# Kernel tuning notes

Hardware: AMD Instinct MI355X
Metric: run time of the kernel (lower is better)

## Reference

```python
import jax, jax.numpy as jnp
import numpy as np

N, D = 16384, 16
EPS = 1e-15
SQRT_C = 1.0            # curvature c = 1 Poincare ball
MAX_NORM = (1.0 - 1e-5) / SQRT_C
ATANH_CLIP = 1.0 - 1e-7


def _proj(x):
    # clip points to stay strictly inside the Poincare ball
    norm = jnp.maximum(jnp.linalg.norm(x, axis=-1, keepdims=True), EPS)
    scale = jnp.where(norm > MAX_NORM, MAX_NORM / norm, 1.0)
    return x * scale


def _logmap0(x):
    # log map at the origin: artanh(sqrt(c)|x|) * x / (sqrt(c)|x|)
    norm = jnp.maximum(jnp.linalg.norm(x, axis=-1, keepdims=True), EPS)
    arg = jnp.minimum(SQRT_C * norm, ATANH_CLIP)
    return jnp.arctanh(arg) * x / (SQRT_C * norm)


def _expmap0(u):
    # exp map at the origin: tanh(sqrt(c)|u|) * u / (sqrt(c)|u|)
    norm = jnp.maximum(jnp.linalg.norm(u, axis=-1, keepdims=True), EPS)
    return jnp.tanh(SQRT_C * norm) * u / (SQRT_C * norm)


def setup_inputs() -> dict:
    key = jax.random.key(0)
    kx, ka = jax.random.split(key)
    # node embeddings strictly inside the unit ball
    x = 0.3 * jax.random.normal(kx, (N, D), dtype=jnp.float32)
    x = _proj(x)
    # dense non-negative adjacency, row-normalized (mean aggregation)
    adj = jax.random.uniform(ka, (N, N), dtype=jnp.float32)
    adj = adj / jnp.sum(adj, axis=-1, keepdims=True)
    return {"x": x, "adj": adj}


def reference(x, adj):
    x_tangent = _logmap0(x)                 # [N, D] pointwise transcendental
    res = jnp.matmul(adj, x_tangent)        # [N, N] @ [N, D] aggregation
    return _proj(_expmap0(res))             # map back to manifold + project
```

## Files before the change

kernel.cpp:

```cpp
#include <hip/hip_runtime.h>
#include <math.h>

#define NROWS 16384
#define DIM   16
#define KC    512
#define NCH   (NROWS / KC)
#define WGT   256
#define RPW   8
#define RPWG  32
#define NT4   (NROWS / 4)

typedef float vfloat4 __attribute__((ext_vector_type(4)));

static __device__ __forceinline__ void fma4(float4& a, float s, const float4& b) {
    a.x = fmaf(s, b.x, a.x);
    a.y = fmaf(s, b.y, a.y);
    a.z = fmaf(s, b.z, a.z);
    a.w = fmaf(s, b.w, a.w);
}
static __device__ __forceinline__ float dot4(const float4& a) {
    return a.x * a.x + a.y * a.y + a.z * a.z + a.w * a.w;
}
static __device__ __forceinline__ float4 scale4(const float4& a, float s) {
    return make_float4(a.x * s, a.y * s, a.z * s, a.w * s);
}

__global__ void hyp_logmap0(const float* __restrict__ x, float4* __restrict__ xtp) {
    int tid = blockIdx.x * blockDim.x + threadIdx.x;
    int s = tid >> 12;
    int t = tid & (NT4 - 1);
    int row = 4 * t + s;
    const float4* src = (const float4*)(x + (size_t)row * DIM);
    float4 q0 = src[0], q1 = src[1], q2 = src[2], q3 = src[3];
    float n2 = dot4(q0) + dot4(q1) + dot4(q2) + dot4(q3);
    float n  = fmaxf(sqrtf(n2), 1e-15f);
    float arg = fminf(n, 1.0f - 1e-7f);
    float f = atanhf(arg) / n;
    xtp[(0 * 4 + s) * NT4 + t] = scale4(q0, f);
    xtp[(1 * 4 + s) * NT4 + t] = scale4(q1, f);
    xtp[(2 * 4 + s) * NT4 + t] = scale4(q2, f);
    xtp[(3 * 4 + s) * NT4 + t] = scale4(q3, f);
}

__global__ __launch_bounds__(WGT, 2) void hyp_agg(
        const float* __restrict__ adj, const float4* __restrict__ xtp,
        float* __restrict__ out) {
    __shared__ float4 planes[2][16][KC / 4];

    const int tid  = threadIdx.x;
    const int lane = tid & 63;
    const int wave = tid >> 6;
    const int rowBase = blockIdx.x * RPWG + wave * RPW;

    const float* a[RPW];
#pragma unroll
    for (int r = 0; r < RPW; ++r)
        a[r] = adj + (size_t)(rowBase + r) * NROWS;

    float4 acc[RPW][4];
#pragma unroll
    for (int r = 0; r < RPW; ++r)
#pragma unroll
        for (int j = 0; j < 4; ++j)
            acc[r][j] = make_float4(0.f, 0.f, 0.f, 0.f);

    auto stage = [&](int buf, int kc) {
#pragma unroll
        for (int i = 0; i < 8; ++i) {
            const int idx = wave * 8 + i;
            const int p   = idx >> 1;
            const int h   = idx & 1;
            const float4* src = xtp + (size_t)p * NT4 + (kc >> 2) + h * 64 + lane;
            __builtin_amdgcn_global_load_lds(
                (const __attribute__((address_space(1))) void*)src,
                (__attribute__((address_space(3))) void*)&planes[buf][p][h * 64],
                16, 0, 0);
        }
    };

    stage(0, 0);
    __syncthreads();

    for (int c = 0; c < NCH; ++c) {
        const int kc  = c * KC;
        const int buf = c & 1;
        if (c + 1 < NCH) stage(buf ^ 1, kc + KC);

#pragma unroll
        for (int it = 0; it < KC / 256; ++it) {
            const int col = kc + it * 256 + 4 * lane;
            vfloat4 v[RPW];
#pragma unroll
            for (int r = 0; r < RPW; ++r)
                v[r] = __builtin_nontemporal_load((const vfloat4*)(a[r] + col));
#pragma unroll
            for (int s = 0; s < 4; ++s) {
                const int t = it * 64 + lane;
                float4 q0 = planes[buf][0 * 4 + s][t];
                float4 q1 = planes[buf][1 * 4 + s][t];
                float4 q2 = planes[buf][2 * 4 + s][t];
                float4 q3 = planes[buf][3 * 4 + s][t];
#pragma unroll
                for (int r = 0; r < RPW; ++r) {
                    float cr = v[r][s];
                    fma4(acc[r][0], cr, q0);
                    fma4(acc[r][1], cr, q1);
                    fma4(acc[r][2], cr, q2);
                    fma4(acc[r][3], cr, q3);
                }
            }
        }
        __syncthreads();
    }

#pragma unroll
    for (int r = 0; r < RPW; ++r) {
#pragma unroll
        for (int j = 0; j < 4; ++j) {
            float4 vv = acc[r][j];
#pragma unroll
            for (int m = 1; m < 64; m <<= 1) {
                vv.x += __shfl_xor(vv.x, m, 64);
                vv.y += __shfl_xor(vv.y, m, 64);
                vv.z += __shfl_xor(vv.z, m, 64);
                vv.w += __shfl_xor(vv.w, m, 64);
            }
            acc[r][j] = vv;
        }
    }

#pragma unroll
    for (int r = 0; r < RPW; ++r) {
        float4 s0 = acc[r][0], s1 = acc[r][1], s2 = acc[r][2], s3 = acc[r][3];
        float n2 = dot4(s0) + dot4(s1) + dot4(s2) + dot4(s3);
        float n  = fmaxf(sqrtf(n2), 1e-15f);
        float t  = tanhf(n);
        float fac = t / n;
        float ny  = fmaxf(t, 1e-15f);
        const float MAX_NORM = 1.0f - 1e-5f;
        float sc  = (ny > MAX_NORM) ? (MAX_NORM / ny) : 1.0f;
        float tot = fac * sc;
        if (lane == 0) {
            float4* dst = (float4*)(out + (size_t)(rowBase + r) * DIM);
            dst[0] = scale4(s0, tot);
            dst[1] = scale4(s1, tot);
            dst[2] = scale4(s2, tot);
            dst[3] = scale4(s3, tot);
        }
    }
}

extern "C" void kernel_launch(void* const* d_in, const int* in_sizes, int n_in,
                              void* d_out, int out_size, void* d_ws, size_t ws_size,
                              hipStream_t stream) {
    const float* x   = (const float*)d_in[0];
    const float* adj = (const float*)d_in[1];
    float* out  = (float*)d_out;
    float4* xtp = (float4*)d_ws;

    hipLaunchKernelGGL(hyp_logmap0, dim3(NROWS / 256), dim3(256), 0, stream, x, xtp);
    hipLaunchKernelGGL(hyp_agg, dim3(NROWS / RPWG), dim3(WGT), 0, stream, adj, xtp, out);
}
```

Before: 248.1 us.

## Store tangent vectors as bf16 and read them directly from global memory

After: 308.9 us. 24.5% more time.

```diff
diff --git a/kernel.cpp b/kernel.cpp
--- a/kernel.cpp
+++ b/kernel.cpp
@@ -1,14 +1,14 @@
 #include <hip/hip_runtime.h>
+#include <hip/hip_bf16.h>
 #include <math.h>
 
 #define NROWS 16384
 #define DIM   16
-#define KC    512
-#define NCH   (NROWS / KC)
-#define WGT   256
-#define RPW   8
+#define WGT   512
+#define RPW   4
 #define RPWG  32
 #define NT4   (NROWS / 4)
+#define NIT   (NROWS / 256)
 
 typedef float vfloat4 __attribute__((ext_vector_type(4)));
 
@@ -24,29 +24,42 @@
 static __device__ __forceinline__ float4 scale4(const float4& a, float s) {
     return make_float4(a.x * s, a.y * s, a.z * s, a.w * s);
 }
+static __device__ __forceinline__ unsigned short bf16r(float v) {
+    union { float f; unsigned u; } c; c.f = v;
+    unsigned r = c.u + 0x7fffu + ((c.u >> 16) & 1u);
+    return (unsigned short)(r >> 16);
+}
+static __device__ __forceinline__ float bf2f(unsigned short h) {
+    union { unsigned u; float f; } c; c.u = ((unsigned)h) << 16;
+    return c.f;
+}
+static __device__ __forceinline__ float4 unpack4(const ushort4& b) {
+    return make_float4(bf2f(b.x), bf2f(b.y), bf2f(b.z), bf2f(b.w));
+}
 
-__global__ void hyp_logmap0(const float* __restrict__ x, float4* __restrict__ xtp) {
+__global__ void hyp_logmap0(const float* __restrict__ x, ushort4* __restrict__ xtb) {
     int tid = blockIdx.x * blockDim.x + threadIdx.x;
     int s = tid >> 12;
     int t = tid & (NT4 - 1);
     int row = 4 * t + s;
     const float4* src = (const float4*)(x + (size_t)row * DIM);
-    float4 q0 = src[0], q1 = src[1], q2 = src[2], q3 = src[3];
-    float n2 = dot4(q0) + dot4(q1) + dot4(q2) + dot4(q3);
+    float4 q[4] = {src[0], src[1], src[2], src[3]};
+    float n2 = dot4(q[0]) + dot4(q[1]) + dot4(q[2]) + dot4(q[3]);
     float n  = fmaxf(sqrtf(n2), 1e-15f);
     float arg = fminf(n, 1.0f - 1e-7f);
     float f = atanhf(arg) / n;
-    xtp[(0 * 4 + s) * NT4 + t] = scale4(q0, f);
-    xtp[(1 * 4 + s) * NT4 + t] = scale4(q1, f);
-    xtp[(2 * 4 + s) * NT4 + t] = scale4(q2, f);
-    xtp[(3 * 4 + s) * NT4 + t] = scale4(q3, f);
+#pragma unroll
+    for (int j = 0; j < 4; ++j) {
+        float4 sq = scale4(q[j], f);
+        ushort4 b;
+        b.x = bf16r(sq.x); b.y = bf16r(sq.y); b.z = bf16r(sq.z); b.w = bf16r(sq.w);
+        xtb[(j * 4 + s) * NT4 + t] = b;
+    }
 }
 
-__global__ __launch_bounds__(WGT, 2) void hyp_agg(
-        const float* __restrict__ adj, const float4* __restrict__ xtp,
+__global__ __launch_bounds__(WGT, 4) void hyp_agg(
+        const float* __restrict__ adj, const ushort4* __restrict__ xtb,
         float* __restrict__ out) {
-    __shared__ float4 planes[2][16][KC / 4];
-
     const int tid  = threadIdx.x;
     const int lane = tid & 63;
     const int wave = tid >> 6;
@@ -64,53 +77,29 @@
         for (int j = 0; j < 4; ++j)
             acc[r][j] = make_float4(0.f, 0.f, 0.f, 0.f);
 
-    auto stage = [&](int buf, int kc) {
+    for (int it = 0; it < NIT; ++it) {
+        const int col  = it * 256 + 4 * lane;
+        const int base = it * 64 + lane;
+        vfloat4 v[RPW];
 #pragma unroll
-        for (int i = 0; i < 8; ++i) {
-            const int idx = wave * 8 + i;
-            const int p   = idx >> 1;
-            const int h   = idx & 1;
-            const float4* src = xtp + (size_t)p * NT4 + (kc >> 2) + h * 64 + lane;
-            __builtin_amdgcn_global_load_lds(
-                (const __attribute__((address_space(1))) void*)src,
-                (__attribute__((address_space(3))) void*)&planes[buf][p][h * 64],
-                16, 0, 0);
-        }
-    };
-
-    stage(0, 0);
-    __syncthreads();
-
-    for (int c = 0; c < NCH; ++c) {
-        const int kc  = c * KC;
-        const int buf = c & 1;
-        if (c + 1 < NCH) stage(buf ^ 1, kc + KC);
-
+        for (int r = 0; r < RPW; ++r)
+            v[r] = __builtin_nontemporal_load((const vfloat4*)(a[r] + col));
 #pragma unroll
-        for (int it = 0; it < KC / 256; ++it) {
-            const int col = kc + it * 256 + 4 * lane;
-            vfloat4 v[RPW];
+        for (int s = 0; s < 4; ++s) {
+            float4 q0 = unpack4(xtb[(0 * 4 + s) * NT4 + base]);
+            float4 q1 = unpack4(xtb[(1 * 4 + s) * NT4 + base]);
+            float4 q2 = unpack4(xtb[(2 * 4 + s) * NT4 + base]);
+            float4 q3 = unpack4(xtb[(3 * 4 + s) * NT4 + base]);
 #pragma unroll
-            for (int r = 0; r < RPW; ++r)
-                v[r] = __builtin_nontemporal_load((const vfloat4*)(a[r] + col));
-#pragma unroll
-            for (int s = 0; s < 4; ++s) {
-                const int t = it * 64 + lane;
-                float4 q0 = planes[buf][0 * 4 + s][t];
-                float4 q1 = planes[buf][1 * 4 + s][t];
-                float4 q2 = planes[buf][2 * 4 + s][t];
-                float4 q3 = planes[buf][3 * 4 + s][t];
-#pragma unroll
-                for (int r = 0; r < RPW; ++r) {
-                    float cr = v[r][s];
-                    fma4(acc[r][0], cr, q0);
-                    fma4(acc[r][1], cr, q1);
-                    fma4(acc[r][2], cr, q2);
-                    fma4(acc[r][3], cr, q3);
-                }
+            for (int r = 0; r < RPW; ++r) {
+                float cr = v[r][s];
+                fma4(acc[r][0], cr, q0);
+                fma4(acc[r][1], cr, q1);
+                fma4(acc[r][2], cr, q2);
+                fma4(acc[r][3], cr, q3);
             }
         }
-        __syncthreads();
+        if ((it & 7) == 7) __builtin_amdgcn_s_barrier();
     }
 
 #pragma unroll
@@ -155,9 +144,9 @@
                               hipStream_t stream) {
     const float* x   = (const float*)d_in[0];
     const float* adj = (const float*)d_in[1];
-    float* out  = (float*)d_out;
-    float4* xtp = (float4*)d_ws;
+    float* out   = (float*)d_out;
+    ushort4* xtb = (ushort4*)d_ws;
 
-    hipLaunchKernelGGL(hyp_logmap0, dim3(NROWS / 256), dim3(256), 0, stream, x, xtp);
-    hipLaunchKernelGGL(hyp_agg, dim3(NROWS / RPWG), dim3(WGT), 0, stream, adj, xtp, out);
+    hipLaunchKernelGGL(hyp_logmap0, dim3(NROWS / 256), dim3(256), 0, stream, x, xtb);
+    hipLaunchKernelGGL(hyp_agg, dim3(NROWS / RPWG), dim3(WGT), 0, stream, adj, xtb, out);
 }
```
